# Kernel tuning notes

Measured on AMD Instinct MI355X. Metric: run time of the kernel, lower is better.

## Reference

```python
import jax, jax.numpy as jnp
import numpy as np

HEADS = 4


def setup_inputs() -> dict:
    key = jax.random.key(0)
    ks = jax.random.split(key, 5)
    B, T, C, H, W = 2, 16, 256, 64, 64
    x = jax.random.normal(ks[0], (B, T, C, H, W), dtype=jnp.float32)
    s = 1.0 / np.sqrt(C).astype(np.float32)  # kaiming-ish init scale for 1x1 conv
    Wq = jax.random.normal(ks[1], (C, C), dtype=jnp.float32) * s
    Wk = jax.random.normal(ks[2], (C, C), dtype=jnp.float32) * s
    Wv = jax.random.normal(ks[3], (C, C), dtype=jnp.float32) * s
    Wp = jax.random.normal(ks[4], (C, C), dtype=jnp.float32) * s
    return {"x": x, "Wq": Wq, "Wk": Wk, "Wv": Wv, "Wp": Wp}


def reference(x, Wq, Wk, Wv, Wp):
    B, T, C, H, W = x.shape
    heads = HEADS
    Ch = C // heads
    scale = Ch ** (-0.5)
    # [B,T,C,H,W] -> [B*H*W, T, C]: each spatial pixel has a T x C temporal track
    xf = jnp.transpose(x, (0, 3, 4, 1, 2)).reshape(B * H * W, T, C)
    # Conv1d(C,C,1,bias=False) == channel matmul: out[n,t,d] = sum_c W[d,c] x[n,t,c]
    q = jnp.einsum('ntc,dc->ntd', xf, Wq).reshape(-1, T, heads, Ch) * scale
    k = jnp.einsum('ntc,dc->ntd', xf, Wk).reshape(-1, T, heads, Ch)
    v = jnp.einsum('ntc,dc->ntd', xf, Wv).reshape(-1, T, heads, Ch)
    k_soft = jax.nn.softmax(k, axis=1)    # softmax over time T (torch dim=-1 of [n,h,c,t])
    q_soft = jax.nn.softmax(q, axis=-1)   # softmax over head channels Ch (torch dim=-2)
    # linear attention: outer-product context then query contraction
    kv = jnp.einsum('nthc,nthd->nhcd', k_soft, v)         # [N,h,Ch,Ch]
    out = jnp.einsum('nthc,nhcd->nthd', q_soft, kv)       # [N,T,h,Ch]
    out = out.reshape(-1, T, C)
    out = jnp.einsum('ntc,dc->ntd', out, Wp)
    out = out.reshape(B, H, W, T, C)
    return jnp.transpose(out, (0, 3, 4, 1, 2))
```

## Files before the change

### kernel.cpp

```cpp
#include <hip/hip_runtime.h>
#include <hip/hip_bf16.h>

#define DI __device__ __forceinline__

typedef __attribute__((ext_vector_type(8))) short bf16x8;
typedef __attribute__((ext_vector_type(4))) float f32x4;
typedef __attribute__((ext_vector_type(4))) _Float16 f16x4;

constexpr float LOG2E = 1.4426950408889634f;

DI float fexp(float x) { return __builtin_amdgcn_exp2f(x * LOG2E); }
DI float frcp(float x) { return __builtin_amdgcn_rcpf(x); }

DI short f2bf(float f) {
  __hip_bfloat16 h = __float2bfloat16(f);
  union { __hip_bfloat16 h; short s; } c; c.h = h; return c.s;
}

DI unsigned pk2(float a, float b) {
  union { __hip_bfloat162 h; unsigned u; } c;
  c.h.x = __float2bfloat16(a); c.h.y = __float2bfloat16(b);
  return c.u;
}

DI short f2h(float f) {
  _Float16 h = (_Float16)f;
  union { _Float16 h; short s; } c; c.h = h; return c.s;
}

DI f16x4 pkh4(float a, float b, float c, float d) {
  auto lo = __builtin_amdgcn_cvt_pkrtz(a, b);
  auto hi = __builtin_amdgcn_cvt_pkrtz(c, d);
  union { struct { decltype(lo) l, h; } p; f16x4 v; } u;
  u.p.l = lo; u.p.h = hi;
  return u.v;
}

DI f16x4 ld4h(const short* p) {
  union { uint2 u; f16x4 v; } c;
  c.u = *(const uint2*)p;
  return c.v;
}

DI f32x4 mfma16(bf16x8 a, bf16x8 b, f32x4 c) {
  return __builtin_amdgcn_mfma_f32_16x16x32_bf16(a, b, c, 0, 0, 0);
}

DI f32x4 mfmah(f16x4 a, f16x4 b, f32x4 c) {
  return __builtin_amdgcn_mfma_f32_16x16x16f16(a, b, c, 0, 0, 0);
}

DI f32x4 fzero() { return f32x4{0.f, 0.f, 0.f, 0.f}; }

DI int xsw(int row, int e) { return row * 256 + (e ^ ((row & 7) << 3)); }

__global__ void wconv_kernel(const float* __restrict__ a, const float* __restrict__ b,
                             const float* __restrict__ c, const float* __restrict__ d,
                             short* __restrict__ o) {
  int i = blockIdx.x * 256 + threadIdx.x;
  int mat = i >> 14;
  int off = (i & 16383) * 4;
  const float* s = (mat == 0) ? a : (mat == 1) ? b : (mat == 2) ? c : d;
  const float sc = (mat == 0) ? 0.125f : 1.0f;
  float4 v = *(const float4*)(s + off);
  uint2 r; r.x = pk2(v.x * sc, v.y * sc); r.y = pk2(v.z * sc, v.w * sc);
  *(uint2*)(o + mat * 65536 + off) = r;
}

__global__ __launch_bounds__(256, 4)
void k1_kernel(const float* __restrict__ x, const short* __restrict__ wbf,
               float* __restrict__ out, short* __restrict__ qsg, int n0chunk) {
  __shared__ short SMEM[16384];
  short* Xs = SMEM;
  short* att_lds = SMEM;

  const int tid  = threadIdx.x;
  const int wave = tid >> 6;
  const int lane = tid & 63;
  const int g    = lane >> 4;
  const int li   = lane & 15;

  int bid = blockIdx.x;
  const int nb = gridDim.x;
  if ((nb & 7) == 0) { const int q = nb >> 3; bid = (bid & 7) * q + (bid >> 3); }

  const int n0  = n0chunk + bid * 4;
  const int b   = n0 >> 12;
  const int hw0 = n0 & 4095;
  const float* xb = x + (size_t)b * (16 * 256 * 4096) + hw0;

  {
    const int c4 = lane;
    #pragma unroll
    for (int it = 0; it < 4; ++it) {
      const int t = it * 4 + wave;
      const float* src = xb + (size_t)(t * 256 + c4 * 4) * 4096;
      float4 v0 = *(const float4*)(src);
      float4 v1 = *(const float4*)(src + 4096);
      float4 v2 = *(const float4*)(src + 8192);
      float4 v3 = *(const float4*)(src + 12288);
      uint2 s0; s0.x = pk2(v0.x, v1.x); s0.y = pk2(v2.x, v3.x);
      uint2 s1; s1.x = pk2(v0.y, v1.y); s1.y = pk2(v2.y, v3.y);
      uint2 s2; s2.x = pk2(v0.z, v1.z); s2.y = pk2(v2.z, v3.z);
      uint2 s3; s3.x = pk2(v0.w, v1.w); s3.y = pk2(v2.w, v3.w);
      *(uint2*)&Xs[xsw(0 * 16 + t, c4 * 4)] = s0;
      *(uint2*)&Xs[xsw(1 * 16 + t, c4 * 4)] = s1;
      *(uint2*)&Xs[xsw(2 * 16 + t, c4 * 4)] = s2;
      *(uint2*)&Xs[xsw(3 * 16 + t, c4 * 4)] = s3;
    }
  }
  __syncthreads();

  const short* wq = wbf;
  const short* wk = wbf + 65536;
  const short* wv = wbf + 131072;
  const size_t wrow = (size_t)(wave * 64) * 256;
  short* qsw = qsg + ((size_t)bid * 4 * 4 + wave) * 1024;

  {
    f32x4 qacc[4][4];
    #pragma unroll
    for (int p = 0; p < 4; ++p)
      #pragma unroll
      for (int nt = 0; nt < 4; ++nt) qacc[p][nt] = fzero();

    __builtin_amdgcn_s_setprio(1);
    #pragma unroll
    for (int ks = 0; ks < 8; ++ks) {
      bf16x8 qb[4];
      #pragma unroll
      for (int nt = 0; nt < 4; ++nt)
        qb[nt] = *(const bf16x8*)(wq + wrow + (size_t)(nt * 16 + li) * 256 + ks * 32 + g * 8);
      #pragma unroll
      for (int p = 0; p < 4; ++p) {
        bf16x8 af = *(const bf16x8*)&Xs[xsw(p * 16 + li, ks * 32 + g * 8)];
        #pragma unroll
        for (int nt = 0; nt < 4; ++nt)
          qacc[p][nt] = mfma16(af, qb[nt], qacc[p][nt]);
      }
    }
    __builtin_amdgcn_s_setprio(0);

    #pragma unroll
    for (int p = 0; p < 4; ++p) {
      short* qsp = qsw + p * 4096;
      #pragma unroll
      for (int r = 0; r < 4; ++r) {
        float e0 = fexp(qacc[p][0][r]);
        float e1 = fexp(qacc[p][1][r]);
        float e2 = fexp(qacc[p][2][r]);
        float e3 = fexp(qacc[p][3][r]);
        float s = e0 + e1 + e2 + e3;
        s += __shfl_xor(s, 1); s += __shfl_xor(s, 2);
        s += __shfl_xor(s, 4); s += __shfl_xor(s, 8);
        const float inv = frcp(s);
        const int t = g * 4 + r;
        short* dst = qsp + t * 64 + li;
        dst[0]  = f2h(e0 * inv);
        dst[16] = f2h(e1 * inv);
        dst[32] = f2h(e2 * inv);
        dst[48] = f2h(e3 * inv);
      }
    }
  }

  f16x4 akf[4][4];
  {
    f32x4 kacc[4][4];
    #pragma unroll
    for (int p = 0; p < 4; ++p)
      #pragma unroll
      for (int nt = 0; nt < 4; ++nt) kacc[p][nt] = fzero();

    __builtin_amdgcn_s_setprio(1);
    #pragma unroll
    for (int ks = 0; ks < 8; ++ks) {
      bf16x8 kb[4];
      #pragma unroll
      for (int nt = 0; nt < 4; ++nt)
        kb[nt] = *(const bf16x8*)(wk + wrow + (size_t)(nt * 16 + li) * 256 + ks * 32 + g * 8);
      #pragma unroll
      for (int p = 0; p < 4; ++p) {
        bf16x8 af = *(const bf16x8*)&Xs[xsw(p * 16 + li, ks * 32 + g * 8)];
        #pragma unroll
        for (int nt = 0; nt < 4; ++nt)
          kacc[p][nt] = mfma16(af, kb[nt], kacc[p][nt]);
      }
    }
    __builtin_amdgcn_s_setprio(0);

    #pragma unroll
    for (int p = 0; p < 4; ++p)
      #pragma unroll
      for (int nt = 0; nt < 4; ++nt) {
        float e0 = fexp(kacc[p][nt][0]);
        float e1 = fexp(kacc[p][nt][1]);
        float e2 = fexp(kacc[p][nt][2]);
        float e3 = fexp(kacc[p][nt][3]);
        float s = e0 + e1 + e2 + e3;
        s += __shfl_xor(s, 16);
        s += __shfl_xor(s, 32);
        const float inv = frcp(s);
        akf[p][nt] = pkh4(e0 * inv, e1 * inv, e2 * inv, e3 * inv);
      }
  }

  f16x4 bvf[4][4];
  #pragma unroll
  for (int h = 0; h < 2; ++h) {
    f32x4 vacc[4][2];
    #pragma unroll
    for (int p = 0; p < 4; ++p)
      #pragma unroll
      for (int n2 = 0; n2 < 2; ++n2) vacc[p][n2] = fzero();

    __builtin_amdgcn_s_setprio(1);
    #pragma unroll
    for (int ks = 0; ks < 8; ++ks) {
      bf16x8 vb[2];
      #pragma unroll
      for (int n2 = 0; n2 < 2; ++n2)
        vb[n2] = *(const bf16x8*)(wv + wrow + (size_t)((h * 2 + n2) * 16 + li) * 256 + ks * 32 + g * 8);
      #pragma unroll
      for (int p = 0; p < 4; ++p) {
        bf16x8 af = *(const bf16x8*)&Xs[xsw(p * 16 + li, ks * 32 + g * 8)];
        #pragma unroll
        for (int n2 = 0; n2 < 2; ++n2)
          vacc[p][n2] = mfma16(af, vb[n2], vacc[p][n2]);
      }
    }
    __builtin_amdgcn_s_setprio(0);

    #pragma unroll
    for (int p = 0; p < 4; ++p)
      #pragma unroll
      for (int n2 = 0; n2 < 2; ++n2)
        bvf[p][h * 2 + n2] = pkh4(vacc[p][n2][0], vacc[p][n2][1],
                                  vacc[p][n2][2], vacc[p][n2][3]);
  }

  asm volatile("s_waitcnt vmcnt(0)" ::: "memory");
  __syncthreads();

  #pragma unroll
  for (int p = 0; p < 4; ++p) {
    const short* qsp = qsw + p * 4096;
    f32x4 oacc[4];
    #pragma unroll
    for (int nt = 0; nt < 4; ++nt) oacc[nt] = fzero();

    #pragma unroll
    for (int cq = 0; cq < 4; ++cq) {
      f32x4 kva[4];
      #pragma unroll
      for (int nt = 0; nt < 4; ++nt)
        kva[nt] = mfmah(akf[p][cq], bvf[p][nt], fzero());
      f16x4 aq = ld4h(qsp + li * 64 + cq * 16 + g * 4);
      #pragma unroll
      for (int nt = 0; nt < 4; ++nt) {
        f16x4 kb16 = pkh4(kva[nt][0], kva[nt][1], kva[nt][2], kva[nt][3]);
        oacc[nt] = mfmah(aq, kb16, oacc[nt]);
      }
    }

    #pragma unroll
    for (int nt = 0; nt < 4; ++nt)
      #pragma unroll
      for (int r = 0; r < 4; ++r) {
        const int row = (g * 4 + r) * 4 + p;
        att_lds[xsw(row, wave * 64 + nt * 16 + li)] = f2bf(oacc[nt][r]);
      }
  }

  __syncthreads();

  {
    const short* wp = wbf + 3 * 65536;
    f32x4 pacc[4][4];
    #pragma unroll
    for (int mt = 0; mt < 4; ++mt)
      #pragma unroll
      for (int n4 = 0; n4 < 4; ++n4) pacc[mt][n4] = fzero();

    __builtin_amdgcn_s_setprio(1);
    #pragma unroll
    for (int ks = 0; ks < 8; ++ks) {
      bf16x8 bw[4];
      #pragma unroll
      for (int n4 = 0; n4 < 4; ++n4)
        bw[n4] = *(const bf16x8*)(wp + (size_t)((wave * 4 + n4) * 16 + li) * 256 + ks * 32 + g * 8);
      #pragma unroll
      for (int mt = 0; mt < 4; ++mt) {
        bf16x8 af = *(const bf16x8*)&att_lds[xsw(mt * 16 + li, ks * 32 + g * 8)];
        #pragma unroll
        for (int n4 = 0; n4 < 4; ++n4)
          pacc[mt][n4] = mfma16(af, bw[n4], pacc[mt][n4]);
      }
    }
    __builtin_amdgcn_s_setprio(0);

    float* ob = out + (size_t)b * (16 * 256 * 4096) + hw0;
    #pragma unroll
    for (int mt = 0; mt < 4; ++mt)
      #pragma unroll
      for (int n4 = 0; n4 < 4; ++n4) {
        const int t = mt * 4 + g;
        const int c = (wave * 4 + n4) * 16 + li;
        float4 v;
        v.x = pacc[mt][n4][0]; v.y = pacc[mt][n4][1];
        v.z = pacc[mt][n4][2]; v.w = pacc[mt][n4][3];
        *(float4*)(ob + (size_t)(t * 256 + c) * 4096) = v;
      }
  }
}

extern "C" void kernel_launch(void* const* d_in, const int* in_sizes, int n_in,
                              void* d_out, int out_size, void* d_ws, size_t ws_size,
                              hipStream_t stream) {
  const float* x  = (const float*)d_in[0];
  const float* Wq = (const float*)d_in[1];
  const float* Wk = (const float*)d_in[2];
  const float* Wv = (const float*)d_in[3];
  const float* Wp = (const float*)d_in[4];
  float* out = (float*)d_out;

  short* wbf = (short*)d_ws;
  short* qsg = wbf + 4 * 65536;

  wconv_kernel<<<256, 256, 0, stream>>>(Wq, Wk, Wv, Wp, wbf);

  const size_t wsAvail = (ws_size > 524288) ? (ws_size - 524288) : 0;
  const size_t perPix = 16 * 256 * 2;
  int chunk = 16;
  while (chunk < 8192 && (size_t)(chunk * 1) * perPix <= wsAvail) chunk <<= 1;

  for (int n0 = 0; n0 < 8192; n0 += chunk) {
    k1_kernel<<<chunk / 4, 256, 0, stream>>>(x, wbf, out, qsg, n0);
  }
}
```

Before: 293.1 us.

## Process sixteen pixels per 1024-thread block for wider coalesced I/O

Each block now handles 16 spatial pixels with 16 waves (4 heads x 4 pixel quads) instead of 4 pixels with 4 waves, so LDS grows to 128KB. Global loads of x and stores of out now cover 16 contiguous floats per row instead of 4, improving coalescing on the strided [B,T,C,H,W] layout. The cost is one block per CU because of the LDS size, which lowers occupancy and latency hiding. The explicit vmcnt wait before the barrier is also removed.

```diff
diff --git a/kernel.cpp b/kernel.cpp
--- a/kernel.cpp
+++ b/kernel.cpp
@@ -67,34 +67,38 @@
   *(uint2*)(o + mat * 65536 + off) = r;
 }
 
-__global__ __launch_bounds__(256, 4)
+__global__ __launch_bounds__(1024, 4)
 void k1_kernel(const float* __restrict__ x, const short* __restrict__ wbf,
                float* __restrict__ out, short* __restrict__ qsg, int n0chunk) {
-  __shared__ short SMEM[16384];
+  __shared__ short SMEM[65536];
   short* Xs = SMEM;
   short* att_lds = SMEM;
 
   const int tid  = threadIdx.x;
-  const int wave = tid >> 6;
+  const int wv   = tid >> 6;
   const int lane = tid & 63;
   const int g    = lane >> 4;
   const int li   = lane & 15;
+  const int head = wv & 3;
+  const int quad = wv >> 2;
 
   int bid = blockIdx.x;
   const int nb = gridDim.x;
   if ((nb & 7) == 0) { const int q = nb >> 3; bid = (bid & 7) * q + (bid >> 3); }
 
-  const int n0  = n0chunk + bid * 4;
+  const int n0  = n0chunk + bid * 16;
   const int b   = n0 >> 12;
   const int hw0 = n0 & 4095;
   const float* xb = x + (size_t)b * (16 * 256 * 4096) + hw0;
 
   {
-    const int c4 = lane;
     #pragma unroll
     for (int it = 0; it < 4; ++it) {
-      const int t = it * 4 + wave;
-      const float* src = xb + (size_t)(t * 256 + c4 * 4) * 4096;
+      const int idx = it * 1024 + tid;
+      const int pq  = idx & 3;
+      const int cq  = (idx >> 2) & 63;
+      const int t   = idx >> 8;
+      const float* src = xb + (size_t)(t * 256 + cq * 4) * 4096 + pq * 4;
       float4 v0 = *(const float4*)(src);
       float4 v1 = *(const float4*)(src + 4096);
       float4 v2 = *(const float4*)(src + 8192);
@@ -103,19 +107,19 @@
       uint2 s1; s1.x = pk2(v0.y, v1.y); s1.y = pk2(v2.y, v3.y);
       uint2 s2; s2.x = pk2(v0.z, v1.z); s2.y = pk2(v2.z, v3.z);
       uint2 s3; s3.x = pk2(v0.w, v1.w); s3.y = pk2(v2.w, v3.w);
-      *(uint2*)&Xs[xsw(0 * 16 + t, c4 * 4)] = s0;
-      *(uint2*)&Xs[xsw(1 * 16 + t, c4 * 4)] = s1;
-      *(uint2*)&Xs[xsw(2 * 16 + t, c4 * 4)] = s2;
-      *(uint2*)&Xs[xsw(3 * 16 + t, c4 * 4)] = s3;
+      *(uint2*)&Xs[xsw((pq * 4 + 0) * 16 + t, cq * 4)] = s0;
+      *(uint2*)&Xs[xsw((pq * 4 + 1) * 16 + t, cq * 4)] = s1;
+      *(uint2*)&Xs[xsw((pq * 4 + 2) * 16 + t, cq * 4)] = s2;
+      *(uint2*)&Xs[xsw((pq * 4 + 3) * 16 + t, cq * 4)] = s3;
     }
   }
   __syncthreads();
 
   const short* wq = wbf;
   const short* wk = wbf + 65536;
-  const short* wv = wbf + 131072;
-  const size_t wrow = (size_t)(wave * 64) * 256;
-  short* qsw = qsg + ((size_t)bid * 4 * 4 + wave) * 1024;
+  const short* wv_ = wbf + 131072;
+  const size_t wrow = (size_t)(head * 64) * 256;
+  short* qsw = qsg + ((size_t)(bid * 16 + quad * 4) * 4 + head) * 1024;
 
   {
     f32x4 qacc[4][4];
@@ -133,7 +137,7 @@
         qb[nt] = *(const bf16x8*)(wq + wrow + (size_t)(nt * 16 + li) * 256 + ks * 32 + g * 8);
       #pragma unroll
       for (int p = 0; p < 4; ++p) {
-        bf16x8 af = *(const bf16x8*)&Xs[xsw(p * 16 + li, ks * 32 + g * 8)];
+        bf16x8 af = *(const bf16x8*)&Xs[xsw((quad * 4 + p) * 16 + li, ks * 32 + g * 8)];
         #pragma unroll
         for (int nt = 0; nt < 4; ++nt)
           qacc[p][nt] = mfma16(af, qb[nt], qacc[p][nt]);
@@ -181,7 +185,7 @@
         kb[nt] = *(const bf16x8*)(wk + wrow + (size_t)(nt * 16 + li) * 256 + ks * 32 + g * 8);
       #pragma unroll
       for (int p = 0; p < 4; ++p) {
-        bf16x8 af = *(const bf16x8*)&Xs[xsw(p * 16 + li, ks * 32 + g * 8)];
+        bf16x8 af = *(const bf16x8*)&Xs[xsw((quad * 4 + p) * 16 + li, ks * 32 + g * 8)];
         #pragma unroll
         for (int nt = 0; nt < 4; ++nt)
           kacc[p][nt] = mfma16(af, kb[nt], kacc[p][nt]);
@@ -220,10 +224,10 @@
       bf16x8 vb[2];
       #pragma unroll
       for (int n2 = 0; n2 < 2; ++n2)
-        vb[n2] = *(const bf16x8*)(wv + wrow + (size_t)((h * 2 + n2) * 16 + li) * 256 + ks * 32 + g * 8);
+        vb[n2] = *(const bf16x8*)(wv_ + wrow + (size_t)((h * 2 + n2) * 16 + li) * 256 + ks * 32 + g * 8);
       #pragma unroll
       for (int p = 0; p < 4; ++p) {
-        bf16x8 af = *(const bf16x8*)&Xs[xsw(p * 16 + li, ks * 32 + g * 8)];
+        bf16x8 af = *(const bf16x8*)&Xs[xsw((quad * 4 + p) * 16 + li, ks * 32 + g * 8)];
         #pragma unroll
         for (int n2 = 0; n2 < 2; ++n2)
           vacc[p][n2] = mfma16(af, vb[n2], vacc[p][n2]);
@@ -239,12 +243,12 @@
                                   vacc[p][n2][2], vacc[p][n2][3]);
   }
 
-  asm volatile("s_waitcnt vmcnt(0)" ::: "memory");
   __syncthreads();
 
   #pragma unroll
   for (int p = 0; p < 4; ++p) {
     const short* qsp = qsw + p * 4096;
+    const int px = quad * 4 + p;
     f32x4 oacc[4];
     #pragma unroll
     for (int nt = 0; nt < 4; ++nt) oacc[nt] = fzero();
@@ -267,8 +271,8 @@
     for (int nt = 0; nt < 4; ++nt)
       #pragma unroll
       for (int r = 0; r < 4; ++r) {
-        const int row = (g * 4 + r) * 4 + p;
-        att_lds[xsw(row, wave * 64 + nt * 16 + li)] = f2bf(oacc[nt][r]);
+        const int row = (g * 4 + r) * 16 + px;
+        att_lds[xsw(row, head * 64 + nt * 16 + li)] = f2bf(oacc[nt][r]);
       }
   }
 
@@ -276,6 +280,8 @@
 
   {
     const short* wp = wbf + 3 * 65536;
+    const int mb = wv >> 2;
+    const int nbt = wv & 3;
     f32x4 pacc[4][4];
     #pragma unroll
     for (int mt = 0; mt < 4; ++mt)
@@ -288,10 +294,10 @@
       bf16x8 bw[4];
       #pragma unroll
       for (int n4 = 0; n4 < 4; ++n4)
-        bw[n4] = *(const bf16x8*)(wp + (size_t)((wave * 4 + n4) * 16 + li) * 256 + ks * 32 + g * 8);
+        bw[n4] = *(const bf16x8*)(wp + (size_t)((nbt * 64 + n4 * 16 + li)) * 256 + ks * 32 + g * 8);
       #pragma unroll
       for (int mt = 0; mt < 4; ++mt) {
-        bf16x8 af = *(const bf16x8*)&att_lds[xsw(mt * 16 + li, ks * 32 + g * 8)];
+        bf16x8 af = *(const bf16x8*)&att_lds[xsw(mb * 64 + mt * 16 + li, ks * 32 + g * 8)];
         #pragma unroll
         for (int n4 = 0; n4 < 4; ++n4)
           pacc[mt][n4] = mfma16(af, bw[n4], pacc[mt][n4]);
@@ -304,12 +310,12 @@
     for (int mt = 0; mt < 4; ++mt)
       #pragma unroll
       for (int n4 = 0; n4 < 4; ++n4) {
-        const int t = mt * 4 + g;
-        const int c = (wave * 4 + n4) * 16 + li;
+        const int t = mb * 4 + mt;
+        const int c = nbt * 64 + n4 * 16 + li;
         float4 v;
         v.x = pacc[mt][n4][0]; v.y = pacc[mt][n4][1];
         v.z = pacc[mt][n4][2]; v.w = pacc[mt][n4][3];
-        *(float4*)(ob + (size_t)(t * 256 + c) * 4096) = v;
+        *(float4*)(ob + (size_t)(t * 256 + c) * 4096 + g * 4) = v;
       }
   }
 }
@@ -335,6 +341,6 @@
   while (chunk < 8192 && (size_t)(chunk * 1) * perPix <= wsAvail) chunk <<= 1;
 
   for (int n0 = 0; n0 < 8192; n0 += chunk) {
-    k1_kernel<<<chunk / 4, 256, 0, stream>>>(x, wbf, out, qsg, n0);
-  }
-}
+    k1_kernel<<<chunk / 16, 1024, 0, stream>>>(x, wbf, out, qsg, n0);
+  }
+}
```

Result: faster. 251.6 us (-14.2%).
